# Optimization experiments

Hardware: AMD Instinct MI355X
Metric: run time of the kernel (lower is better)

## Reference

```python
import jax, jax.numpy as jnp
import numpy as np

X_SCALE, X_ZP = 0.03, -66      # int8 quant params (qmin=-128, qmax=127)
Y_SCALE, Y_ZP = 0.025, 160     # uint8 quant params (qmin=0, qmax=255)
M = K = N = 4096


def setup_inputs() -> dict:
    key = jax.random.key(0)
    kx, ky = jax.random.split(key)
    # x holds int8-range values [-128, 127], y holds uint8-range values [0, 255]
    x = jax.random.randint(kx, (M, K), -128, 128, dtype=jnp.int32)
    y = jax.random.randint(ky, (K, N), 0, 256, dtype=jnp.int32)
    return {"x": x, "y": y}


def reference(x, y):
    # dequantize_per_tensor: (q - zero_point) * scale  (values already in [qmin, qmax])
    xf = (x.astype(jnp.float32) - X_ZP) * X_SCALE   # [M, K]
    yf = (y.astype(jnp.float32) - Y_ZP) * Y_SCALE   # [K, N]
    return jnp.matmul(xf, yf)                       # [M, N]
```

## Files before the change

kernel.cpp:

```cpp
#include <hip/hip_runtime.h>
#include <stdint.h>

#define Mdim 4096
#define Kdim 4096
#define Ndim 4096

typedef __attribute__((ext_vector_type(4))) int v4i;
typedef __attribute__((ext_vector_type(16))) int v16i;

__device__ __forceinline__ void gload_lds16(const void* g, void* l) {
  __builtin_amdgcn_global_load_lds(
      (__attribute__((address_space(1))) void*)(uintptr_t)g,
      (__attribute__((address_space(3))) void*)(uint32_t)(uintptr_t)l,
      16, 0, 0);
}

__global__ __launch_bounds__(256) void pack_x_kernel(const int* __restrict__ x,
                                                     char* __restrict__ x8,
                                                     int* __restrict__ rsx) {
  const int row = blockIdx.x;
  const int t = threadIdx.x;
  const int4* src = (const int4*)(x + (size_t)row * Kdim);
  int* dst = (int*)(x8 + (size_t)row * Kdim);
  int sum = 0;
#pragma unroll
  for (int i = 0; i < 4; ++i) {
    int4 v = src[t + 256 * i];
    sum += v.x + v.y + v.z + v.w;
    dst[t + 256 * i] =
        (v.x & 0xff) | ((v.y & 0xff) << 8) | ((v.z & 0xff) << 16) | (v.w << 24);
  }
#pragma unroll
  for (int o = 32; o > 0; o >>= 1) sum += __shfl_down(sum, o, 64);
  __shared__ int red[4];
  if ((t & 63) == 0) red[t >> 6] = sum;
  __syncthreads();
  if (t == 0) rsx[row] = red[0] + red[1] + red[2] + red[3];
}

__global__ __launch_bounds__(256) void pack_yt_kernel(const int* __restrict__ y,
                                                      char* __restrict__ yt,
                                                      int* __restrict__ csy) {
  __shared__ int wt[64 * 17];
  const int t = threadIdx.x;
  const int n0 = blockIdx.x * 64;
  const int k0 = blockIdx.y * 64;
  const int c = t & 15;
  const int r0 = t >> 4;
#pragma unroll
  for (int s = 0; s < 4; ++s) {
    const int r = r0 + s * 16;
    int4 v = *(const int4*)(y + (size_t)(k0 + r) * Ndim + n0 + c * 4);
    v.x -= 128; v.y -= 128; v.z -= 128; v.w -= 128;
    wt[r * 17 + c] =
        (v.x & 0xff) | ((v.y & 0xff) << 8) | ((v.z & 0xff) << 16) | (v.w << 24);
  }
  __syncthreads();
  const int n = t >> 2;
  const int kq = t & 3;
  const int colw = n >> 2;
  const int byi = (n & 3) * 8;
  int outw[4];
  int bsum = 0;
#pragma unroll
  for (int j = 0; j < 4; ++j) {
    int b[4];
#pragma unroll
    for (int jj = 0; jj < 4; ++jj) {
      const int word = wt[(kq * 16 + j * 4 + jj) * 17 + colw];
      b[jj] = (word >> byi) & 0xff;
      bsum += (int)(char)b[jj];
    }
    outw[j] = b[0] | (b[1] << 8) | (b[2] << 16) | (b[3] << 24);
  }
  *(int4*)(yt + (size_t)(n0 + n) * Kdim + k0 + kq * 16) =
      make_int4(outw[0], outw[1], outw[2], outw[3]);
  bsum += __shfl_xor(bsum, 1, 64);
  bsum += __shfl_xor(bsum, 2, 64);
  if (kq == 0) atomicAdd(csy + n0 + n, bsum);
}

__global__ __launch_bounds__(256, 2) void gemm_i8_kernel(
    const char* __restrict__ A, const char* __restrict__ B,
    const int* __restrict__ rsx, const int* __restrict__ csy,
    float* __restrict__ out) {
  __shared__ __align__(16) char lds[2 * 24576];
  const int t = threadIdx.x;
  const int l = t & 63;
  const int w = t >> 6;
  const int bm = blockIdx.y * 256;
  const int bn = blockIdx.x * 128;

  v16i acc[2][4];
#pragma unroll
  for (int i = 0; i < 2; ++i)
#pragma unroll
    for (int j = 0; j < 4; ++j)
#pragma unroll
      for (int q = 0; q < 16; ++q) acc[i][j][q] = 0;

  const int srow = t >> 2;
  const int cswz = ((t & 3) ^ ((t >> 3) & 3)) * 16;
  const char* gA = A + (size_t)(bm + srow) * Kdim + cswz;
  const char* gB = B + (size_t)(bn + srow) * Kdim + cswz;

#define STAGE(buf_off, koff)                                                  \
  do {                                                                        \
    _Pragma("unroll") for (int i = 0; i < 4; ++i)                             \
        gload_lds16(gA + (koff) + (size_t)i * 64 * Kdim,                      \
                    lds + (buf_off) + i * 4096 + t * 16);                     \
    _Pragma("unroll") for (int i = 0; i < 2; ++i)                             \
        gload_lds16(gB + (koff) + (size_t)i * 64 * Kdim,                      \
                    lds + (buf_off) + 16384 + i * 4096 + t * 16);             \
  } while (0)

  const int arow = w * 64 + (l & 31);
  const int brow = l & 31;
  const int lhalf = l >> 5;
  const int lkey = (l >> 1) & 3;

#define COMPUTE_HALF(buf_off, ks)                                             \
  do {                                                                        \
    const char* As = lds + (buf_off);                                         \
    const char* Bs = lds + (buf_off) + 16384;                                 \
    const int slot = (((ks) * 2 + lhalf) ^ lkey) * 16;                        \
    v4i a[2], b[4];                                                           \
    _Pragma("unroll") for (int i = 0; i < 2; ++i)                             \
        a[i] = *(const v4i*)(As + (arow + i * 32) * 64 + slot);               \
    _Pragma("unroll") for (int j = 0; j < 4; ++j)                             \
        b[j] = *(const v4i*)(Bs + (brow + j * 32) * 64 + slot);               \
    _Pragma("unroll") for (int i = 0; i < 2; ++i)                             \
        _Pragma("unroll") for (int j = 0; j < 4; ++j)                         \
            acc[i][j] = __builtin_amdgcn_mfma_i32_32x32x32_i8(                \
                a[i], b[j], acc[i][j], 0, 0, 0);                              \
  } while (0)

  const int ksA = w & 1;

  STAGE(0, 0);
  __syncthreads();
  for (int kt = 0; kt < 64; kt += 2) {
    COMPUTE_HALF(0, ksA);
    STAGE(24576, (kt + 1) * 64);
    COMPUTE_HALF(0, ksA ^ 1);
    __syncthreads();
    COMPUTE_HALF(24576, ksA);
    if (kt + 2 < 64) STAGE(0, (kt + 2) * 64);
    COMPUTE_HALF(24576, ksA ^ 1);
    __syncthreads();
  }

  const int col = l & 31;
#pragma unroll
  for (int i = 0; i < 2; ++i) {
    const int gm0 = bm + w * 64 + i * 32;
#pragma unroll
    for (int j = 0; j < 4; ++j) {
      const int gn = bn + j * 32 + col;
      const int cs = 66 * csy[gn] - 8650752;
#pragma unroll
      for (int r = 0; r < 16; ++r) {
        const int row = (r & 3) + 8 * (r >> 2) + 4 * lhalf;
        const int gm = gm0 + row;
        const int val = acc[i][j][r] - 32 * rsx[gm] + cs;
        out[(size_t)gm * Ndim + gn] = 7.5e-4f * (float)val;
      }
    }
  }
#undef STAGE
#undef COMPUTE_HALF
}

extern "C" void kernel_launch(void* const* d_in, const int* in_sizes, int n_in,
                              void* d_out, int out_size, void* d_ws, size_t ws_size,
                              hipStream_t stream) {
  (void)in_sizes; (void)n_in; (void)out_size; (void)ws_size;
  const int* x = (const int*)d_in[0];
  const int* y = (const int*)d_in[1];
  float* out = (float*)d_out;
  char* ws = (char*)d_ws;
  char* x8 = ws;
  char* yt = ws + (size_t)Mdim * Kdim;
  int* rsx = (int*)(ws + (size_t)Mdim * Kdim + (size_t)Kdim * Ndim);
  int* csy = rsx + Mdim;

  hipMemsetAsync(csy, 0, Ndim * sizeof(int), stream);
  pack_x_kernel<<<Mdim, 256, 0, stream>>>(x, x8, rsx);
  pack_yt_kernel<<<dim3(Ndim / 64, Kdim / 64), 256, 0, stream>>>(y, yt, csy);
  gemm_i8_kernel<<<dim3(Ndim / 128, Mdim / 256), 256, 0, stream>>>(x8, yt, rsx, csy, out);
}
```

Before: 247.9 us.

## Rewrite Y pack/transpose with byte-perm transpose and partial column sums

The Y pack kernel now has each block loop over eight 64-wide K tiles. It transposes 4x4 byte blocks in registers with perm instructions and uses a swizzled LDS layout, so each 16-byte row write to yt is a single vector store. Column sums are computed with sdot4 and written as 8 per-K-slice partials rather than through atomicAdd, which also removes the memset launch. The GEMM epilogue then sums the 8 partials per column, adding a few extra global loads per thread.

```diff
diff --git a/kernel.cpp b/kernel.cpp
--- a/kernel.cpp
+++ b/kernel.cpp
@@ -13,6 +13,19 @@
       (__attribute__((address_space(1))) void*)(uintptr_t)g,
       (__attribute__((address_space(3))) void*)(uint32_t)(uintptr_t)l,
       16, 0, 0);
+}
+
+__device__ __forceinline__ int bytesum_i8(int w, int acc) {
+#if __has_builtin(__builtin_amdgcn_sdot4)
+  return __builtin_amdgcn_sdot4(w, 0x01010101, acc, false);
+#else
+  return acc + (int)(char)(w) + (int)(char)(w >> 8) + (int)(char)(w >> 16) +
+         (w >> 24);
+#endif
+}
+
+__device__ __forceinline__ int pack4(int4 v) {
+  return (v.x & 0xff) | ((v.y & 0xff) << 8) | ((v.z & 0xff) << 16) | (v.w << 24);
 }
 
 __global__ __launch_bounds__(256) void pack_x_kernel(const int* __restrict__ x,
@@ -27,8 +40,7 @@
   for (int i = 0; i < 4; ++i) {
     int4 v = src[t + 256 * i];
     sum += v.x + v.y + v.z + v.w;
-    dst[t + 256 * i] =
-        (v.x & 0xff) | ((v.y & 0xff) << 8) | ((v.z & 0xff) << 16) | (v.w << 24);
+    dst[t + 256 * i] = pack4(v);
   }
 #pragma unroll
   for (int o = 32; o > 0; o >>= 1) sum += __shfl_down(sum, o, 64);
@@ -40,49 +52,72 @@
 
 __global__ __launch_bounds__(256) void pack_yt_kernel(const int* __restrict__ y,
                                                       char* __restrict__ yt,
-                                                      int* __restrict__ csy) {
-  __shared__ int wt[64 * 17];
+                                                      int* __restrict__ csp) {
+  __shared__ int wt[64 * 20];
+  __shared__ int psum[4 * 64];
   const int t = threadIdx.x;
   const int n0 = blockIdx.x * 64;
-  const int k0 = blockIdx.y * 64;
-  const int c = t & 15;
-  const int r0 = t >> 4;
-#pragma unroll
-  for (int s = 0; s < 4; ++s) {
-    const int r = r0 + s * 16;
-    int4 v = *(const int4*)(y + (size_t)(k0 + r) * Ndim + n0 + c * 4);
-    v.x -= 128; v.y -= 128; v.z -= 128; v.w -= 128;
-    wt[r * 17 + c] =
-        (v.x & 0xff) | ((v.y & 0xff) << 8) | ((v.z & 0xff) << 16) | (v.w << 24);
+  const int kbase = blockIdx.y * 512;
+  const int w = t >> 6;
+  const int u = t & 63;
+  const int nq = u & 15;
+  const int kq = w * 4 + (u >> 4);
+  const int n_p2 = t >> 2;
+  const int g = t & 3;
+  const int key1 = (nq >> 1) & 3;
+  const int key2 = (n_p2 >> 3) & 3;
+  int csum[4] = {0, 0, 0, 0};
+
+  for (int kt = 0; kt < 8; ++kt) {
+    const int k0 = kbase + kt * 64;
+    const int* srcp = y + (size_t)(k0 + kq * 4) * Ndim + n0 + nq * 4;
+    int4 v0 = *(const int4*)(srcp);
+    int4 v1 = *(const int4*)(srcp + Ndim);
+    int4 v2 = *(const int4*)(srcp + 2 * Ndim);
+    int4 v3 = *(const int4*)(srcp + 3 * Ndim);
+    const int a0 = pack4(v0) ^ (int)0x80808080;
+    const int a1 = pack4(v1) ^ (int)0x80808080;
+    const int a2 = pack4(v2) ^ (int)0x80808080;
+    const int a3 = pack4(v3) ^ (int)0x80808080;
+    const unsigned x01l = __builtin_amdgcn_perm(a1, a0, 0x05010400u);
+    const unsigned x01h = __builtin_amdgcn_perm(a1, a0, 0x07030602u);
+    const unsigned x23l = __builtin_amdgcn_perm(a3, a2, 0x05010400u);
+    const unsigned x23h = __builtin_amdgcn_perm(a3, a2, 0x07030602u);
+    int wo[4];
+    wo[0] = (int)__builtin_amdgcn_perm(x23l, x01l, 0x05040100u);
+    wo[1] = (int)__builtin_amdgcn_perm(x23l, x01l, 0x07060302u);
+    wo[2] = (int)__builtin_amdgcn_perm(x23h, x01h, 0x05040100u);
+    wo[3] = (int)__builtin_amdgcn_perm(x23h, x01h, 0x07060302u);
+#pragma unroll
+    for (int i = 0; i < 4; ++i) {
+      csum[i] = bytesum_i8(wo[i], csum[i]);
+      const int n = nq * 4 + i;
+      wt[n * 20 + (((kq >> 2) ^ key1) * 4) + (kq & 3)] = wo[i];
+    }
+    __syncthreads();
+    v4i wv = *(const v4i*)(wt + n_p2 * 20 + (g ^ key2) * 4);
+    *(v4i*)(yt + (size_t)(n0 + n_p2) * Kdim + k0 + g * 16) = wv;
+    __syncthreads();
+  }
+#pragma unroll
+  for (int i = 0; i < 4; ++i) {
+    csum[i] += __shfl_xor(csum[i], 16, 64);
+    csum[i] += __shfl_xor(csum[i], 32, 64);
+  }
+  if (u < 16) {
+#pragma unroll
+    for (int i = 0; i < 4; ++i) psum[w * 64 + u * 4 + i] = csum[i];
   }
   __syncthreads();
-  const int n = t >> 2;
-  const int kq = t & 3;
-  const int colw = n >> 2;
-  const int byi = (n & 3) * 8;
-  int outw[4];
-  int bsum = 0;
-#pragma unroll
-  for (int j = 0; j < 4; ++j) {
-    int b[4];
-#pragma unroll
-    for (int jj = 0; jj < 4; ++jj) {
-      const int word = wt[(kq * 16 + j * 4 + jj) * 17 + colw];
-      b[jj] = (word >> byi) & 0xff;
-      bsum += (int)(char)b[jj];
-    }
-    outw[j] = b[0] | (b[1] << 8) | (b[2] << 16) | (b[3] << 24);
-  }
-  *(int4*)(yt + (size_t)(n0 + n) * Kdim + k0 + kq * 16) =
-      make_int4(outw[0], outw[1], outw[2], outw[3]);
-  bsum += __shfl_xor(bsum, 1, 64);
-  bsum += __shfl_xor(bsum, 2, 64);
-  if (kq == 0) atomicAdd(csy + n0 + n, bsum);
+  if (t < 64) {
+    const int tot = psum[t] + psum[64 + t] + psum[128 + t] + psum[192 + t];
+    csp[blockIdx.y * Ndim + n0 + t] = tot;
+  }
 }
 
 __global__ __launch_bounds__(256, 2) void gemm_i8_kernel(
     const char* __restrict__ A, const char* __restrict__ B,
-    const int* __restrict__ rsx, const int* __restrict__ csy,
+    const int* __restrict__ rsx, const int* __restrict__ csp,
     float* __restrict__ out) {
   __shared__ __align__(16) char lds[2 * 24576];
   const int t = threadIdx.x;
@@ -151,18 +186,26 @@
   }
 
   const int col = l & 31;
+  int csj[4];
+#pragma unroll
+  for (int j = 0; j < 4; ++j) {
+    const int gn = bn + j * 32 + col;
+    int s = 0;
+#pragma unroll
+    for (int p = 0; p < 8; ++p) s += csp[p * Ndim + gn];
+    csj[j] = 66 * s - 8650752;
+  }
 #pragma unroll
   for (int i = 0; i < 2; ++i) {
     const int gm0 = bm + w * 64 + i * 32;
 #pragma unroll
     for (int j = 0; j < 4; ++j) {
       const int gn = bn + j * 32 + col;
-      const int cs = 66 * csy[gn] - 8650752;
 #pragma unroll
       for (int r = 0; r < 16; ++r) {
         const int row = (r & 3) + 8 * (r >> 2) + 4 * lhalf;
         const int gm = gm0 + row;
-        const int val = acc[i][j][r] - 32 * rsx[gm] + cs;
+        const int val = acc[i][j][r] - 32 * rsx[gm] + csj[j];
         out[(size_t)gm * Ndim + gn] = 7.5e-4f * (float)val;
       }
     }
@@ -182,10 +225,9 @@
   char* x8 = ws;
   char* yt = ws + (size_t)Mdim * Kdim;
   int* rsx = (int*)(ws + (size_t)Mdim * Kdim + (size_t)Kdim * Ndim);
-  int* csy = rsx + Mdim;
-
-  hipMemsetAsync(csy, 0, Ndim * sizeof(int), stream);
+  int* csp = rsx + Mdim;
+
   pack_x_kernel<<<Mdim, 256, 0, stream>>>(x, x8, rsx);
-  pack_yt_kernel<<<dim3(Ndim / 64, Kdim / 64), 256, 0, stream>>>(y, yt, csy);
-  gemm_i8_kernel<<<dim3(Ndim / 128, Mdim / 256), 256, 0, stream>>>(x8, yt, rsx, csy, out);
-}
+  pack_yt_kernel<<<dim3(Ndim / 64, 8), 256, 0, stream>>>(y, yt, csp);
+  gemm_i8_kernel<<<dim3(Ndim / 128, Mdim / 256), 256, 0, stream>>>(x8, yt, rsx, csp, out);
+}
```

Result: no change. 248.9 us (+0.4%).
